# Optimization experiments

Hardware: AMD Instinct MI355X
Metric: run time of the kernel (lower is better)

The kernel has to match this reference:

```python
import jax, jax.numpy as jnp
import numpy as np

F_SIZE = 32
H_DIM = 540
W_DIM = 960
T_DIM = 300
HID1 = 64
FEAT = 64
HID2X2 = 256
UV_L = 10
T_L = 6
BLOCK2_IN = FEAT + (UV_L * 2 * 2 + 2) + (T_L * 2 + 1)  # 119
N_PTS = 1048576


def plane_sample(plane, uv):
    """Bilinear grid_sample, align_corners=False, padding_mode='border'.
    plane: (f, H, W); uv: (N, 2) in [0,1]; uv[:,0] samples W, uv[:,1] samples H
    (matches torch grid last-dim (x, y) convention). Returns (N, f)."""
    f, H, W = plane.shape
    g = uv * 2.0 - 1.0
    u, v = g[:, 0], g[:, 1]
    # unnormalize (align_corners=False) then border-clamp the coordinate
    ix = jnp.clip(((u + 1.0) * W - 1.0) * 0.5, 0.0, W - 1.0)
    iy = jnp.clip(((v + 1.0) * H - 1.0) * 0.5, 0.0, H - 1.0)
    x0f = jnp.floor(ix)
    y0f = jnp.floor(iy)
    wx = ix - x0f
    wy = iy - y0f
    x0 = x0f.astype(jnp.int32)
    y0 = y0f.astype(jnp.int32)
    x1 = jnp.minimum(x0 + 1, W - 1)
    y1 = jnp.minimum(y0 + 1, H - 1)
    v00 = plane[:, y0, x0]  # (f, N)
    v01 = plane[:, y0, x1]
    v10 = plane[:, y1, x0]
    v11 = plane[:, y1, x1]
    out = (v00 * (1 - wx) * (1 - wy) + v01 * wx * (1 - wy)
           + v10 * (1 - wx) * wy + v11 * wx * wy)
    return out.T  # (N, f)


def pos_enc(x, L):
    outs = [x]
    for j in range(L):
        s = (2.0 ** j) * x
        outs.append(jnp.sin(s))
        outs.append(jnp.cos(s))
    return jnp.concatenate(outs, axis=-1)


def _linear_params(key, fan_in, fan_out):
    kw, kb = jax.random.split(key)
    scale = 1.0 / np.sqrt(fan_in)
    W = jax.random.uniform(kw, (fan_in, fan_out), minval=-scale, maxval=scale, dtype=jnp.float32)
    b = jax.random.uniform(kb, (fan_out,), minval=-scale, maxval=scale, dtype=jnp.float32)
    return W, b


def setup_inputs() -> dict:
    key = jax.random.key(0)
    ks = jax.random.split(key, 10)
    xyt = jax.random.uniform(ks[0], (N_PTS, 3), dtype=jnp.float32)
    xyt = xyt.at[:, 2].multiply(300.0)  # t in [0, frames_num)
    yx_plane = jax.random.uniform(ks[1], (F_SIZE, H_DIM, W_DIM), dtype=jnp.float32)
    xt_plane = jax.random.uniform(ks[2], (F_SIZE, W_DIM, T_DIM), dtype=jnp.float32)
    yt_plane = jax.random.uniform(ks[3], (F_SIZE, H_DIM, T_DIM), dtype=jnp.float32)
    fw1, fb1 = _linear_params(ks[4], F_SIZE, HID1)
    fw2, fb2 = _linear_params(ks[5], HID1, FEAT)
    w1, b1 = _linear_params(ks[6], BLOCK2_IN, HID2X2)
    w2, b2 = _linear_params(ks[7], HID2X2, HID2X2)
    w3, b3 = _linear_params(ks[8], HID2X2, HID2X2)
    w4, b4 = _linear_params(ks[9], HID2X2, 3)
    return {"xyt": xyt, "yx_plane": yx_plane, "xt_plane": xt_plane,
            "yt_plane": yt_plane, "fw1": fw1, "fb1": fb1, "fw2": fw2,
            "fb2": fb2, "w1": w1, "b1": b1, "w2": w2, "b2": b2,
            "w3": w3, "b3": b3, "w4": w4, "b4": b4, "frames_num": 300}


def reference(xyt, yx_plane, xt_plane, yt_plane, fw1, fb1, fw2, fb2,
              w1, b1, w2, b2, w3, b3, w4, b4, frames_num):
    x = xyt[:, 0:1]
    y = xyt[:, 1:2]
    t = xyt[:, 2:3] / frames_num
    yx_f = plane_sample(yx_plane, jnp.concatenate([y, x], axis=-1))
    xt_f = plane_sample(xt_plane, jnp.concatenate([x, t], axis=-1))
    yt_f = plane_sample(yt_plane, jnp.concatenate([y, t], axis=-1))
    feat = yx_f * xt_f * yt_f  # (N, f_size)
    h = jax.nn.relu(feat @ fw1 + fb1)
    h = jax.nn.relu(h @ fw2 + fb2)
    yx_pe = pos_enc(jnp.concatenate([y, x], axis=-1), UV_L)
    t_pe = pos_enc(t, T_L)
    full = jnp.concatenate([h, yx_pe, t_pe], axis=-1)  # (N, 119)
    z = jax.nn.relu(full @ w1 + b1)
    z = jax.nn.relu(z @ w2 + b2)
    z = jax.nn.relu(z @ w3 + b3)
    colors = jax.nn.sigmoid(z @ w4 + b4)  # (N, 3)
    return colors
```

## Files before the change

kernel.cpp:

```cpp
#include <hip/hip_runtime.h>

typedef __bf16 bf16_t;
typedef __bf16 bf16x8 __attribute__((ext_vector_type(8)));
typedef _Float16 f16x4 __attribute__((ext_vector_type(4)));
typedef unsigned short u16x8 __attribute__((ext_vector_type(8)));
typedef unsigned short u16x4 __attribute__((ext_vector_type(4)));
typedef float f32x4 __attribute__((ext_vector_type(4)));

#define MT 64
#define NTHR 512
#define NBLK (1048576 / MT)

__device__ __forceinline__ int fragoff(int NK, int pg, int n, int p15) {
  return ((pg * NK + (n >> 5)) << 10) + (((n >> 3) & 3) << 8) + (p15 << 4) + ((n & 7) << 1);
}
__device__ __forceinline__ void st_frag1(char* buf, int NK, int pg, int n, int p15, float v) {
  *reinterpret_cast<unsigned short*>(buf + fragoff(NK, pg, n, p15)) =
      __builtin_bit_cast(unsigned short, (bf16_t)v);
}
__device__ __forceinline__ void st_frag4(char* buf, int NK, int pg, int n, int p15, float v0,
                                         float v1, float v2, float v3) {
  u16x4 pk;
  pk[0] = __builtin_bit_cast(unsigned short, (bf16_t)v0);
  pk[1] = __builtin_bit_cast(unsigned short, (bf16_t)v1);
  pk[2] = __builtin_bit_cast(unsigned short, (bf16_t)v2);
  pk[3] = __builtin_bit_cast(unsigned short, (bf16_t)v3);
  *reinterpret_cast<uint2*>(buf + fragoff(NK, pg, n, p15)) = __builtin_bit_cast(uint2, pk);
}

__global__ void KPlanes_tr3(const float* __restrict__ yx, const float* __restrict__ xt,
                            const float* __restrict__ yt, uint4* __restrict__ d0,
                            uint4* __restrict__ d1, uint4* __restrict__ d2) {
  const int HW0 = 518400, HW1 = 288000, HW2 = 162000;
  const int NB0 = 2025, NB1 = 1125;
  const int b = blockIdx.x;
  const float* src;
  uint4* dst;
  int HW, s;
  if (b < NB0) {
    src = yx; dst = d0; HW = HW0; s = b * 256 + threadIdx.x;
  } else if (b < NB0 + NB1) {
    src = xt; dst = d1; HW = HW1; s = (b - NB0) * 256 + threadIdx.x;
  } else {
    src = yt; dst = d2; HW = HW2; s = (b - NB0 - NB1) * 256 + threadIdx.x;
  }
  if (s >= HW) return;
#pragma unroll
  for (int g = 0; g < 4; ++g) {
    u16x8 v;
#pragma unroll
    for (int j = 0; j < 8; ++j) {
      const float w = src[(size_t)(g * 8 + j) * HW + s];
      v[j] = __builtin_bit_cast(unsigned short, (_Float16)w);
    }
    dst[(size_t)s * 4 + g] = __builtin_bit_cast(uint4, v);
  }
}

__global__ void KPlanes_packall(const float* __restrict__ fw1, const float* __restrict__ fw2,
                                const float* __restrict__ w1, const float* __restrict__ w2,
                                const float* __restrict__ w3, const float* __restrict__ w4,
                                uint4* __restrict__ dst) {
  const int F = blockIdx.x * 4 + (threadIdx.x >> 6);
  const int lane = threadIdx.x & 63;
  if (F >= 340) return;
  const float* W;
  int N, K, KS, fbase;
  if (F < 4)        { W = fw1; N = 64;  K = 32;  KS = 1; fbase = 0; }
  else if (F < 12)  { W = fw2; N = 64;  K = 64;  KS = 2; fbase = 4; }
  else if (F < 76)  { W = w1;  N = 256; K = 119; KS = 4; fbase = 12; }
  else if (F < 204) { W = w2;  N = 256; K = 256; KS = 8; fbase = 76; }
  else if (F < 332) { W = w3;  N = 256; K = 256; KS = 8; fbase = 204; }
  else              { W = w4;  N = 3;   K = 256; KS = 8; fbase = 332; }
  const int f = F - fbase;
  const int g = f / KS, ks = f - g * KS;
  const int col = g * 16 + (lane & 15);
  u16x8 v;
#pragma unroll
  for (int j = 0; j < 8; ++j) {
    const int k = ks * 32 + (lane >> 4) * 8 + j;
    const float w = (k < K && col < N) ? W[(size_t)k * N + col] : 0.0f;
    v[j] = __builtin_bit_cast(unsigned short, (bf16_t)w);
  }
  dst[(size_t)F * 64 + lane] = __builtin_bit_cast(uint4, v);
}

struct Smp4 {
  uint2 c00, c01, c10, c11;
  float w00, w01, w10, w11;
};
__device__ __forceinline__ Smp4 sample_ld4(const uint2* __restrict__ plt, int Hd, int Wd, float u,
                                           float v, int q) {
  Smp4 s;
  float ix = fminf(fmaxf(u * (float)Wd - 0.5f, 0.f), (float)Wd - 1.f);
  float iy = fminf(fmaxf(v * (float)Hd - 0.5f, 0.f), (float)Hd - 1.f);
  float x0f = floorf(ix), y0f = floorf(iy);
  float wx = ix - x0f, wy = iy - y0f;
  int x0 = (int)x0f, y0 = (int)y0f;
  int x1 = min(x0 + 1, Wd - 1), y1 = min(y0 + 1, Hd - 1);
  s.w00 = (1.f - wx) * (1.f - wy);
  s.w01 = wx * (1.f - wy);
  s.w10 = (1.f - wx) * wy;
  s.w11 = wx * wy;
  const size_t r0 = (size_t)y0 * Wd, r1 = (size_t)y1 * Wd;
  s.c00 = plt[(r0 + x0) * 8 + q];
  s.c01 = plt[(r0 + x1) * 8 + q];
  s.c10 = plt[(r1 + x0) * 8 + q];
  s.c11 = plt[(r1 + x1) * 8 + q];
  return s;
}
__device__ __forceinline__ void smp_combine4(const Smp4& s, float* o) {
  const f16x4 a = __builtin_bit_cast(f16x4, s.c00);
  const f16x4 b = __builtin_bit_cast(f16x4, s.c01);
  const f16x4 c = __builtin_bit_cast(f16x4, s.c10);
  const f16x4 d = __builtin_bit_cast(f16x4, s.c11);
#pragma unroll
  for (int i = 0; i < 4; ++i)
    o[i] = (float)a[i] * s.w00 + (float)b[i] * s.w01 + (float)c[i] * s.w10 + (float)d[i] * s.w11;
}

template <int KS, int NKOUT, int NT, int MTPW, bool RELU>
__device__ __forceinline__ void layer_fp(const char* in, char* outb, const uint4* __restrict__ Wf,
                                         const float* __restrict__ bg, int gbase, int moff,
                                         int lane) {
  const int l15 = lane & 15, lhi = lane >> 4;
  const char* rb = in + lane * 16 + moff * (KS << 10);
  f32x4 acc[MTPW][NT];
#pragma unroll
  for (int m = 0; m < MTPW; ++m)
#pragma unroll
    for (int t = 0; t < NT; ++t) acc[m][t] = f32x4{0.f, 0.f, 0.f, 0.f};
#pragma unroll
  for (int ks = 0; ks < KS; ++ks) {
    bf16x8 wa[NT];
#pragma unroll
    for (int t = 0; t < NT; ++t)
      wa[t] = __builtin_bit_cast(bf16x8, Wf[(size_t)((gbase + t) * KS + ks) * 64 + lane]);
#pragma unroll
    for (int m = 0; m < MTPW; ++m) {
      const uint4 u = *reinterpret_cast<const uint4*>(rb + ((m * KS + ks) << 10));
      const bf16x8 b = __builtin_bit_cast(bf16x8, u);
#pragma unroll
      for (int t = 0; t < NT; ++t)
        acc[m][t] = __builtin_amdgcn_mfma_f32_16x16x32_bf16(wa[t], b, acc[m][t], 0, 0, 0);
    }
  }
#pragma unroll
  for (int t = 0; t < NT; ++t) {
    const int ncol = (gbase + t) * 16 + lhi * 4;
    const float4 bb = *reinterpret_cast<const float4*>(&bg[ncol]);
#pragma unroll
    for (int m = 0; m < MTPW; ++m) {
      float v0 = acc[m][t][0] + bb.x, v1 = acc[m][t][1] + bb.y;
      float v2 = acc[m][t][2] + bb.z, v3 = acc[m][t][3] + bb.w;
      if (RELU) {
        v0 = fmaxf(v0, 0.f); v1 = fmaxf(v1, 0.f);
        v2 = fmaxf(v2, 0.f); v3 = fmaxf(v3, 0.f);
      }
      st_frag4(outb, NKOUT, moff + m, ncol, l15, v0, v1, v2, v3);
    }
  }
}

__global__ __launch_bounds__(NTHR, 4) void KPlanes_fused7(
    const float* __restrict__ xyt, const uint2* __restrict__ yx_h, const uint2* __restrict__ xt_h,
    const uint2* __restrict__ yt_h, const uint4* __restrict__ wf1, const float* __restrict__ fb1,
    const uint4* __restrict__ wf2, const float* __restrict__ fb2, const uint4* __restrict__ wf3,
    const float* __restrict__ b1, const uint4* __restrict__ wf4, const float* __restrict__ b2,
    const uint4* __restrict__ wf5, const float* __restrict__ b3, const uint4* __restrict__ wf6,
    const float* __restrict__ b4, const int* __restrict__ fnum_p, float* __restrict__ out) {
  __shared__ char actS[32768];
  __shared__ char actB[32768];
  const int tid = threadIdx.x;
  const int lane = tid & 63;
  const int wid = tid >> 6;
  const float rfn = 1.0f / (float)(*fnum_p);

  {
    const int p = tid >> 3;
    const int q = tid & 7;
    const int pg = p >> 4, p15 = p & 15;
    const int pgl = blockIdx.x * MT + p;
    const float x = xyt[pgl * 3 + 0];
    const float y = xyt[pgl * 3 + 1];
    const float t = xyt[pgl * 3 + 2] * rfn;
    Smp4 sYX = sample_ld4(yx_h, 540, 960, y, x, q);
    Smp4 sXT = sample_ld4(xt_h, 960, 300, x, t, q);
    Smp4 sYT = sample_ld4(yt_h, 540, 300, y, t, q);
    if (q == 4) {
      st_frag1(actS, 4, pg, 64, p15, y);
      float sj, cj;
      sincosf(y, &sj, &cj);
#pragma unroll
      for (int j = 0; j < 10; ++j) {
        st_frag1(actS, 4, pg, 66 + j * 4, p15, sj);
        st_frag1(actS, 4, pg, 68 + j * 4, p15, cj);
        const float ns = 2.f * sj * cj;
        cj = fmaf(-2.f * sj, sj, 1.f);
        sj = ns;
      }
    } else if (q == 5) {
      st_frag1(actS, 4, pg, 65, p15, x);
      float sj, cj;
      sincosf(x, &sj, &cj);
#pragma unroll
      for (int j = 0; j < 10; ++j) {
        st_frag1(actS, 4, pg, 67 + j * 4, p15, sj);
        st_frag1(actS, 4, pg, 69 + j * 4, p15, cj);
        const float ns = 2.f * sj * cj;
        cj = fmaf(-2.f * sj, sj, 1.f);
        sj = ns;
      }
    } else if (q == 6) {
      st_frag1(actS, 4, pg, 106, p15, t);
      float sj, cj;
      sincosf(t, &sj, &cj);
#pragma unroll
      for (int j = 0; j < 6; ++j) {
        st_frag1(actS, 4, pg, 107 + 2 * j, p15, sj);
        st_frag1(actS, 4, pg, 108 + 2 * j, p15, cj);
        const float ns = 2.f * sj * cj;
        cj = fmaf(-2.f * sj, sj, 1.f);
        sj = ns;
      }
    } else if (q == 7) {
      st_frag1(actS, 4, pg, 119, p15, 0.f);
      *reinterpret_cast<uint4*>(actS + fragoff(4, pg, 120, p15)) = uint4{0u, 0u, 0u, 0u};
    }
    float a4[4], b4_[4], c4[4];
    smp_combine4(sYX, a4);
    smp_combine4(sXT, b4_);
    smp_combine4(sYT, c4);
    st_frag4(actS + 16384, 1, pg, q * 4, p15, a4[0] * b4_[0] * c4[0], a4[1] * b4_[1] * c4[1],
             a4[2] * b4_[2] * c4[2], a4[3] * b4_[3] * c4[3]);
  }
  __syncthreads();
  layer_fp<1, 2, 1, 2, true>(actS + 16384, actB, wf1, fb1, wid & 3, (wid >> 2) * 2, lane);
  __syncthreads();
  layer_fp<2, 4, 1, 2, true>(actB, actS, wf2, fb2, wid & 3, (wid >> 2) * 2, lane);
  __syncthreads();
  layer_fp<4, 8, 2, 4, true>(actS, actB, wf3, b1, wid * 2, 0, lane);
  __syncthreads();
  layer_fp<8, 8, 2, 4, true>(actB, actS, wf4, b2, wid * 2, 0, lane);
  __syncthreads();
  layer_fp<8, 8, 2, 4, true>(actS, actB, wf5, b3, wid * 2, 0, lane);
  __syncthreads();
  if (wid < 4) {
    const int l15 = lane & 15, lhi = lane >> 4;
    const char* rb = actB + lane * 16 + wid * 8192;
    f32x4 acc = {0.f, 0.f, 0.f, 0.f};
#pragma unroll
    for (int ks = 0; ks < 8; ++ks) {
      const bf16x8 wa = __builtin_bit_cast(bf16x8, wf6[ks * 64 + lane]);
      const bf16x8 b = __builtin_bit_cast(bf16x8, *reinterpret_cast<const uint4*>(rb + (ks << 10)));
      acc = __builtin_amdgcn_mfma_f32_16x16x32_bf16(wa, b, acc, 0, 0, 0);
    }
    if (lhi == 0) {
      const size_t pgl = (size_t)blockIdx.x * MT + wid * 16 + l15;
#pragma unroll
      for (int i = 0; i < 3; ++i) {
        const float v = acc[i] + b4[i];
        out[pgl * 3 + i] = 1.f / (1.f + expf(-v));
      }
    }
  }
}

__device__ __forceinline__ int swz(int row, int colbyte) {
  return row * 512 + (colbyte ^ ((row & 31) << 4));
}
__device__ __forceinline__ void st_act(unsigned short* buf, int row, int col, float v) {
  buf[swz(row, col * 2) >> 1] = __builtin_bit_cast(unsigned short, (bf16_t)v);
}
__device__ __forceinline__ bf16x8 ld_frag(const unsigned short* buf, int row, int kbyte) {
  const uint4 u =
      *reinterpret_cast<const uint4*>(reinterpret_cast<const char*>(buf) + swz(row, kbyte));
  return __builtin_bit_cast(bf16x8, u);
}
__device__ __forceinline__ void sample8_f(const float* __restrict__ pl, int Hd, int Wd, float u,
                                          float v, int cgrp, float* o) {
  float ix = fminf(fmaxf(u * (float)Wd - 0.5f, 0.f), (float)Wd - 1.f);
  float iy = fminf(fmaxf(v * (float)Hd - 0.5f, 0.f), (float)Hd - 1.f);
  float x0f = floorf(ix), y0f = floorf(iy);
  float wx = ix - x0f, wy = iy - y0f;
  int x0 = (int)x0f, y0 = (int)y0f;
  int x1 = min(x0 + 1, Wd - 1), y1 = min(y0 + 1, Hd - 1);
  float w00 = (1.f - wx) * (1.f - wy), w01 = wx * (1.f - wy);
  float w10 = (1.f - wx) * wy, w11 = wx * wy;
  const size_t HW = (size_t)Hd * Wd;
#pragma unroll
  for (int i = 0; i < 8; ++i) {
    const float* bc = pl + (size_t)(cgrp + i) * HW;
    float a = bc[(size_t)y0 * Wd + x0], b = bc[(size_t)y0 * Wd + x1];
    float c = bc[(size_t)y1 * Wd + x0], d = bc[(size_t)y1 * Wd + x1];
    o[i] = a * w00 + b * w01 + c * w10 + d * w11;
  }
}

template <int KSTEPS, int NCPW, bool RELU>
__device__ __forceinline__ void mfma_layer_fb(const unsigned short* inb, unsigned short* outb,
                                              const float* __restrict__ Wg,
                                              const float* __restrict__ bg, int N, int Kmax,
                                              int wid, int lane) {
  const int l15 = lane & 15;
  const int lhi = lane >> 4;
#pragma unroll
  for (int t = 0; t < NCPW; ++t) {
    const int nc = wid * NCPW + t;
    const int col = nc * 16 + l15;
    const float bias = bg[col];
    bf16x8 bfrag[KSTEPS];
#pragma unroll
    for (int ks = 0; ks < KSTEPS; ++ks) {
#pragma unroll
      for (int j = 0; j < 8; ++j) {
        const int k = ks * 32 + lhi * 8 + j;
        float wv = (k < Kmax) ? Wg[(size_t)k * N + col] : 0.0f;
        bfrag[ks][j] = (bf16_t)wv;
      }
    }
#pragma unroll
    for (int m = 0; m < 4; ++m) {
      f32x4 acc = {0.f, 0.f, 0.f, 0.f};
#pragma unroll
      for (int ks = 0; ks < KSTEPS; ++ks) {
        bf16x8 a = ld_frag(inb, m * 16 + l15, ks * 64 + lhi * 16);
        acc = __builtin_amdgcn_mfma_f32_16x16x32_bf16(a, bfrag[ks], acc, 0, 0, 0);
      }
      const int r0 = m * 16 + lhi * 4;
#pragma unroll
      for (int i = 0; i < 4; ++i) {
        float v = acc[i] + bias;
        if (RELU) v = fmaxf(v, 0.f);
        st_act(outb, r0 + i, col, v);
      }
    }
  }
}

__global__ __launch_bounds__(256) void KPlanes_fused_fb(
    const float* __restrict__ xyt, const float* __restrict__ yx, const float* __restrict__ xt,
    const float* __restrict__ yt, const float* __restrict__ fw1, const float* __restrict__ fb1,
    const float* __restrict__ fw2, const float* __restrict__ fb2, const float* __restrict__ w1,
    const float* __restrict__ b1, const float* __restrict__ w2, const float* __restrict__ b2,
    const float* __restrict__ w3, const float* __restrict__ b3, const float* __restrict__ w4,
    const float* __restrict__ b4, const int* __restrict__ fnum_p, float* __restrict__ out) {
  __shared__ unsigned short actA[64 * 256];
  __shared__ unsigned short actB[64 * 256];
  const int tid = threadIdx.x;
  const int lane = tid & 63;
  const int wid = tid >> 6;
  const float fnum = (float)(*fnum_p);
  {
    const int p = tid >> 2;
    const int cgrp = (tid & 3) * 8;
    const int pg = blockIdx.x * 64 + p;
    float x = xyt[pg * 3 + 0];
    float y = xyt[pg * 3 + 1];
    float t = xyt[pg * 3 + 2] / fnum;
    float syx[8], sxt[8], syt[8];
    sample8_f(yx, 540, 960, y, x, cgrp, syx);
    sample8_f(xt, 960, 300, x, t, cgrp, sxt);
    sample8_f(yt, 540, 300, y, t, cgrp, syt);
#pragma unroll
    for (int i = 0; i < 8; ++i) st_act(actA, p, cgrp + i, syx[i] * sxt[i] * syt[i]);
  }
  __syncthreads();
  mfma_layer_fb<1, 1, true>(actA, actB, fw1, fb1, 64, 32, wid, lane);
  __syncthreads();
  mfma_layer_fb<2, 1, true>(actB, actA, fw2, fb2, 64, 64, wid, lane);
  if (tid < 64) {
    const int pg = blockIdx.x * 64 + tid;
    float px = xyt[pg * 3 + 0];
    float py = xyt[pg * 3 + 1];
    float pt = xyt[pg * 3 + 2] / fnum;
    st_act(actA, tid, 64, py);
    st_act(actA, tid, 65, px);
    float sc = 1.f;
#pragma unroll
    for (int j = 0; j < 10; ++j) {
      st_act(actA, tid, 66 + j * 4 + 0, sinf(sc * py));
      st_act(actA, tid, 66 + j * 4 + 1, sinf(sc * px));
      st_act(actA, tid, 66 + j * 4 + 2, cosf(sc * py));
      st_act(actA, tid, 66 + j * 4 + 3, cosf(sc * px));
      sc *= 2.f;
    }
    st_act(actA, tid, 106, pt);
    sc = 1.f;
#pragma unroll
    for (int j = 0; j < 6; ++j) {
      st_act(actA, tid, 107 + j * 2, sinf(sc * pt));
      st_act(actA, tid, 108 + j * 2, cosf(sc * pt));
      sc *= 2.f;
    }
#pragma unroll
    for (int c = 119; c < 128; ++c) st_act(actA, tid, c, 0.f);
  }
  __syncthreads();
  mfma_layer_fb<4, 4, true>(actA, actB, w1, b1, 256, 119, wid, lane);
  __syncthreads();
  mfma_layer_fb<8, 4, true>(actB, actA, w2, b2, 256, 256, wid, lane);
  __syncthreads();
  mfma_layer_fb<8, 4, true>(actA, actB, w3, b3, 256, 256, wid, lane);
  __syncthreads();
  {
    const int p = tid >> 2, c = tid & 3;
    if (c < 3) {
      float acc = 0.f;
#pragma unroll
      for (int k0 = 0; k0 < 256; k0 += 8) {
        int b = swz(p, k0 * 2);
        uint4 u = *reinterpret_cast<const uint4*>(reinterpret_cast<const char*>(actB) + b);
        bf16x8 z = __builtin_bit_cast(bf16x8, u);
#pragma unroll
        for (int j = 0; j < 8; ++j) acc += (float)z[j] * w4[(k0 + j) * 3 + c];
      }
      acc += b4[c];
      out[(size_t)(blockIdx.x * 64 + p) * 3 + c] = 1.f / (1.f + expf(-acc));
    }
  }
}

extern "C" void kernel_launch(void* const* d_in, const int* in_sizes, int n_in, void* d_out,
                              int out_size, void* d_ws, size_t ws_size, hipStream_t stream) {
  const float* xyt = (const float*)d_in[0];
  const float* yx = (const float*)d_in[1];
  const float* xt = (const float*)d_in[2];
  const float* yt = (const float*)d_in[3];
  const float* fw1 = (const float*)d_in[4];
  const float* fb1 = (const float*)d_in[5];
  const float* fw2 = (const float*)d_in[6];
  const float* fb2 = (const float*)d_in[7];
  const float* w1 = (const float*)d_in[8];
  const float* b1 = (const float*)d_in[9];
  const float* w2 = (const float*)d_in[10];
  const float* b2 = (const float*)d_in[11];
  const float* w3 = (const float*)d_in[12];
  const float* b3 = (const float*)d_in[13];
  const float* w4 = (const float*)d_in[14];
  const float* b4 = (const float*)d_in[15];
  const int* fnum = (const int*)d_in[16];
  float* out = (float*)d_out;

  const int hw_yx = 540 * 960, hw_xt = 960 * 300, hw_yt = 540 * 300;
  const size_t plane_bytes = ((size_t)hw_yx + hw_xt + hw_yt) * 64;
  const size_t wfrag_bytes = (size_t)340 * 64 * sizeof(uint4);
  const size_t need = plane_bytes + wfrag_bytes;

  char* ws = (char*)d_ws;
  uint2* yx_h = (uint2*)ws;
  uint2* xt_h = (uint2*)(ws + (size_t)hw_yx * 64);
  uint2* yt_h = (uint2*)(ws + (size_t)(hw_yx + hw_xt) * 64);
  uint4* wbase = (uint4*)(ws + plane_bytes);
  uint4* wf1 = wbase + 0 * 64;
  uint4* wf2 = wbase + 4 * 64;
  uint4* wf3 = wbase + 12 * 64;
  uint4* wf4 = wbase + 76 * 64;
  uint4* wf5 = wbase + 204 * 64;
  uint4* wf6 = wbase + 332 * 64;

  if (ws_size >= need) {
    const int nb_tr = 2025 + 1125 + 633;
    KPlanes_tr3<<<nb_tr, 256, 0, stream>>>(yx, xt, yt, (uint4*)yx_h, (uint4*)xt_h, (uint4*)yt_h);
    KPlanes_packall<<<85, 256, 0, stream>>>(fw1, fw2, w1, w2, w3, w4, wbase);
    KPlanes_fused7<<<NBLK, NTHR, 0, stream>>>(xyt, yx_h, xt_h, yt_h, wf1, fb1, wf2, fb2, wf3, b1,
                                              wf4, b2, wf5, b3, wf6, b4, fnum, out);
  } else {
    KPlanes_fused_fb<<<1048576 / 64, 256, 0, stream>>>(xyt, yx, xt, yt, fw1, fb1, fw2, fb2, w1,
                                                       b1, w2, b2, w3, b3, w4, b4, fnum, out);
  }
}
```

Before: 477.2 us.

## Halve LDS with in-place MLP layers to raise occupancy

Merges the two 32KB shared activation buffers into one 32KB buffer. The three wide layers now compute in place: each wave accumulates in registers, hits a barrier, then writes its outputs over the input. The work split is also changed so each wave owns one 16-point group and half of the output columns. Launch bounds go from 4 to 6 blocks per CU, trading extra register pressure and more barriers for higher occupancy to hide the latency of the gathers.

```diff
diff --git a/kernel.cpp b/kernel.cpp
--- a/kernel.cpp
+++ b/kernel.cpp
@@ -162,15 +162,49 @@
   }
 }
 
-__global__ __launch_bounds__(NTHR, 4) void KPlanes_fused7(
+template <int KS, bool RELU>
+__device__ __forceinline__ void layer_ipf(char* Zb, int inoff, const uint4* __restrict__ Wf,
+                                          const float* __restrict__ bg, int wid, int lane) {
+  const int l15 = lane & 15, lhi = lane >> 4;
+  const int pg = wid >> 1, nh = wid & 1;
+  const char* rb = Zb + inoff + pg * (KS << 10) + lane * 16;
+  const uint4* wp = Wf + (size_t)(nh * 8) * KS * 64 + lane;
+  f32x4 acc[8];
+#pragma unroll
+  for (int t = 0; t < 8; ++t) acc[t] = f32x4{0.f, 0.f, 0.f, 0.f};
+#pragma unroll
+  for (int ks = 0; ks < KS; ++ks) {
+    const bf16x8 b = __builtin_bit_cast(bf16x8, *reinterpret_cast<const uint4*>(rb + (ks << 10)));
+#pragma unroll
+    for (int t = 0; t < 8; ++t) {
+      const bf16x8 wa = __builtin_bit_cast(bf16x8, wp[(size_t)(t * KS + ks) * 64]);
+      acc[t] = __builtin_amdgcn_mfma_f32_16x16x32_bf16(wa, b, acc[t], 0, 0, 0);
+    }
+  }
+  __syncthreads();
+#pragma unroll
+  for (int t = 0; t < 8; ++t) {
+    const int ncol = (nh * 8 + t) * 16 + lhi * 4;
+    const float4 bb = *reinterpret_cast<const float4*>(&bg[ncol]);
+    float v0 = acc[t][0] + bb.x, v1 = acc[t][1] + bb.y;
+    float v2 = acc[t][2] + bb.z, v3 = acc[t][3] + bb.w;
+    if (RELU) {
+      v0 = fmaxf(v0, 0.f); v1 = fmaxf(v1, 0.f);
+      v2 = fmaxf(v2, 0.f); v3 = fmaxf(v3, 0.f);
+    }
+    st_frag4(Zb, 8, pg, ncol, l15, v0, v1, v2, v3);
+  }
+  __syncthreads();
+}
+
+__global__ __launch_bounds__(NTHR, 6) void KPlanes_fused8(
     const float* __restrict__ xyt, const uint2* __restrict__ yx_h, const uint2* __restrict__ xt_h,
     const uint2* __restrict__ yt_h, const uint4* __restrict__ wf1, const float* __restrict__ fb1,
     const uint4* __restrict__ wf2, const float* __restrict__ fb2, const uint4* __restrict__ wf3,
     const float* __restrict__ b1, const uint4* __restrict__ wf4, const float* __restrict__ b2,
     const uint4* __restrict__ wf5, const float* __restrict__ b3, const uint4* __restrict__ wf6,
     const float* __restrict__ b4, const int* __restrict__ fnum_p, float* __restrict__ out) {
-  __shared__ char actS[32768];
-  __shared__ char actB[32768];
+  __shared__ char Z[32768];
   const int tid = threadIdx.x;
   const int lane = tid & 63;
   const int wid = tid >> 6;
@@ -187,67 +221,65 @@
     Smp4 sYX = sample_ld4(yx_h, 540, 960, y, x, q);
     Smp4 sXT = sample_ld4(xt_h, 960, 300, x, t, q);
     Smp4 sYT = sample_ld4(yt_h, 540, 300, y, t, q);
+    char* pe = Z + 8192;
     if (q == 4) {
-      st_frag1(actS, 4, pg, 64, p15, y);
+      st_frag1(pe, 4, pg, 64, p15, y);
       float sj, cj;
       sincosf(y, &sj, &cj);
 #pragma unroll
       for (int j = 0; j < 10; ++j) {
-        st_frag1(actS, 4, pg, 66 + j * 4, p15, sj);
-        st_frag1(actS, 4, pg, 68 + j * 4, p15, cj);
+        st_frag1(pe, 4, pg, 66 + j * 4, p15, sj);
+        st_frag1(pe, 4, pg, 68 + j * 4, p15, cj);
         const float ns = 2.f * sj * cj;
         cj = fmaf(-2.f * sj, sj, 1.f);
         sj = ns;
       }
     } else if (q == 5) {
-      st_frag1(actS, 4, pg, 65, p15, x);
+      st_frag1(pe, 4, pg, 65, p15, x);
       float sj, cj;
       sincosf(x, &sj, &cj);
 #pragma unroll
       for (int j = 0; j < 10; ++j) {
-        st_frag1(actS, 4, pg, 67 + j * 4, p15, sj);
-        st_frag1(actS, 4, pg, 69 + j * 4, p15, cj);
+        st_frag1(pe, 4, pg, 67 + j * 4, p15, sj);
+        st_frag1(pe, 4, pg, 69 + j * 4, p15, cj);
         const float ns = 2.f * sj * cj;
         cj = fmaf(-2.f * sj, sj, 1.f);
         sj = ns;
       }
     } else if (q == 6) {
-      st_frag1(actS, 4, pg, 106, p15, t);
+      st_frag1(pe, 4, pg, 106, p15, t);
       float sj, cj;
       sincosf(t, &sj, &cj);
 #pragma unroll
       for (int j = 0; j < 6; ++j) {
-        st_frag1(actS, 4, pg, 107 + 2 * j, p15, sj);
-        st_frag1(actS, 4, pg, 108 + 2 * j, p15, cj);
+        st_frag1(pe, 4, pg, 107 + 2 * j, p15, sj);
+        st_frag1(pe, 4, pg, 108 + 2 * j, p15, cj);
         const float ns = 2.f * sj * cj;
         cj = fmaf(-2.f * sj, sj, 1.f);
         sj = ns;
       }
     } else if (q == 7) {
-      st_frag1(actS, 4, pg, 119, p15, 0.f);
-      *reinterpret_cast<uint4*>(actS + fragoff(4, pg, 120, p15)) = uint4{0u, 0u, 0u, 0u};
+      st_frag1(pe, 4, pg, 119, p15, 0.f);
+      *reinterpret_cast<uint4*>(pe + fragoff(4, pg, 120, p15)) = uint4{0u, 0u, 0u, 0u};
     }
     float a4[4], b4_[4], c4[4];
     smp_combine4(sYX, a4);
     smp_combine4(sXT, b4_);
     smp_combine4(sYT, c4);
-    st_frag4(actS + 16384, 1, pg, q * 4, p15, a4[0] * b4_[0] * c4[0], a4[1] * b4_[1] * c4[1],
+    st_frag4(Z + 28672, 1, pg, q * 4, p15, a4[0] * b4_[0] * c4[0], a4[1] * b4_[1] * c4[1],
              a4[2] * b4_[2] * c4[2], a4[3] * b4_[3] * c4[3]);
   }
   __syncthreads();
-  layer_fp<1, 2, 1, 2, true>(actS + 16384, actB, wf1, fb1, wid & 3, (wid >> 2) * 2, lane);
-  __syncthreads();
-  layer_fp<2, 4, 1, 2, true>(actB, actS, wf2, fb2, wid & 3, (wid >> 2) * 2, lane);
-  __syncthreads();
-  layer_fp<4, 8, 2, 4, true>(actS, actB, wf3, b1, wid * 2, 0, lane);
-  __syncthreads();
-  layer_fp<8, 8, 2, 4, true>(actB, actS, wf4, b2, wid * 2, 0, lane);
-  __syncthreads();
-  layer_fp<8, 8, 2, 4, true>(actS, actB, wf5, b3, wid * 2, 0, lane);
-  __syncthreads();
+  layer_fp<1, 2, 1, 2, true>(Z + 28672, Z, wf1, fb1, wid & 3, (wid >> 2) * 2, lane);
+  __syncthreads();
+  layer_fp<2, 4, 1, 2, true>(Z, Z + 8192, wf2, fb2, wid & 3, (wid >> 2) * 2, lane);
+  __syncthreads();
+  layer_ipf<4, true>(Z, 8192, wf3, b1, wid, lane);
+  layer_ipf<8, true>(Z, 0, wf4, b2, wid, lane);
+  layer_ipf<8, true>(Z, 0, wf5, b3, wid, lane);
   if (wid < 4) {
     const int l15 = lane & 15, lhi = lane >> 4;
-    const char* rb = actB + lane * 16 + wid * 8192;
+    const char* rb = Z + lane * 16 + wid * 8192;
     f32x4 acc = {0.f, 0.f, 0.f, 0.f};
 #pragma unroll
     for (int ks = 0; ks < 8; ++ks) {
@@ -463,7 +495,7 @@
     const int nb_tr = 2025 + 1125 + 633;
     KPlanes_tr3<<<nb_tr, 256, 0, stream>>>(yx, xt, yt, (uint4*)yx_h, (uint4*)xt_h, (uint4*)yt_h);
     KPlanes_packall<<<85, 256, 0, stream>>>(fw1, fw2, w1, w2, w3, w4, wbase);
-    KPlanes_fused7<<<NBLK, NTHR, 0, stream>>>(xyt, yx_h, xt_h, yt_h, wf1, fb1, wf2, fb2, wf3, b1,
+    KPlanes_fused8<<<NBLK, NTHR, 0, stream>>>(xyt, yx_h, xt_h, yt_h, wf1, fb1, wf2, fb2, wf3, b1,
                                               wf4, b2, wf5, b3, wf6, b4, fnum, out);
   } else {
     KPlanes_fused_fb<<<1048576 / 64, 256, 0, stream>>>(xyt, yx, xt, yt, fw1, fb1, fw2, fb2, w1,
```

Measured after the change: 1.227 ms. +157.2%, slower.

## Make fused kernel loop over tiles and prefetch next tile's plane samples

Applied to the files above, without the earlier changes.

The fused kernel becomes semi-persistent: each block processes 32 consecutive 64-point tiles instead of one. It issues the plane gathers for the next tile, and the coordinate loads for the tile after that, before running the current tile's MLP layers. The aim is to hide gather latency behind the MFMA work and to amortize block launch and setup. In exchange the grid drops to 512 blocks, which may leave CU slots idle given the 4-blocks-per-CU launch bound. Holding the sample state across the layers also adds register pressure.

```diff
diff --git a/kernel.cpp b/kernel.cpp
--- a/kernel.cpp
+++ b/kernel.cpp
@@ -9,7 +9,8 @@
 
 #define MT 64
 #define NTHR 512
-#define NBLK (1048576 / MT)
+#define TPB 32
+#define NPBLK (1048576 / (MT * TPB))
 
 __device__ __forceinline__ int fragoff(int NK, int pg, int n, int p15) {
   return ((pg * NK + (n >> 5)) << 10) + (((n >> 3) & 3) << 8) + (p15 << 4) + ((n & 7) << 1);
@@ -162,7 +163,7 @@
   }
 }
 
-__global__ __launch_bounds__(NTHR, 4) void KPlanes_fused7(
+__global__ __launch_bounds__(NTHR, 4) void KPlanes_fusedP(
     const float* __restrict__ xyt, const uint2* __restrict__ yx_h, const uint2* __restrict__ xt_h,
     const uint2* __restrict__ yt_h, const uint4* __restrict__ wf1, const float* __restrict__ fb1,
     const uint4* __restrict__ wf2, const float* __restrict__ fb2, const uint4* __restrict__ wf3,
@@ -175,18 +176,37 @@
   const int lane = tid & 63;
   const int wid = tid >> 6;
   const float rfn = 1.0f / (float)(*fnum_p);
-
+  const int p = tid >> 3, q = tid & 7;
+  const int pg = p >> 4, p15 = p & 15;
+  const int tbase = blockIdx.x * TPB;
+
+  float x, y, t, xn, yn, tn;
   {
-    const int p = tid >> 3;
-    const int q = tid & 7;
-    const int pg = p >> 4, p15 = p & 15;
-    const int pgl = blockIdx.x * MT + p;
-    const float x = xyt[pgl * 3 + 0];
-    const float y = xyt[pgl * 3 + 1];
-    const float t = xyt[pgl * 3 + 2] * rfn;
-    Smp4 sYX = sample_ld4(yx_h, 540, 960, y, x, q);
-    Smp4 sXT = sample_ld4(xt_h, 960, 300, x, t, q);
-    Smp4 sYT = sample_ld4(yt_h, 540, 300, y, t, q);
+    const int p0 = tbase * MT + p;
+    x = xyt[p0 * 3 + 0];
+    y = xyt[p0 * 3 + 1];
+    t = xyt[p0 * 3 + 2] * rfn;
+  }
+  Smp4 sYX = sample_ld4(yx_h, 540, 960, y, x, q);
+  Smp4 sXT = sample_ld4(xt_h, 960, 300, x, t, q);
+  Smp4 sYT = sample_ld4(yt_h, 540, 300, y, t, q);
+  {
+    const int p1 = (tbase + 1) * MT + p;
+    xn = xyt[p1 * 3 + 0];
+    yn = xyt[p1 * 3 + 1];
+    tn = xyt[p1 * 3 + 2] * rfn;
+  }
+
+#pragma unroll 1
+  for (int it = 0; it < TPB; ++it) {
+    {
+      float a4[4], b4_[4], c4[4];
+      smp_combine4(sYX, a4);
+      smp_combine4(sXT, b4_);
+      smp_combine4(sYT, c4);
+      st_frag4(actS + 16384, 1, pg, q * 4, p15, a4[0] * b4_[0] * c4[0], a4[1] * b4_[1] * c4[1],
+               a4[2] * b4_[2] * c4[2], a4[3] * b4_[3] * c4[3]);
+    }
     if (q == 4) {
       st_frag1(actS, 4, pg, 64, p15, y);
       float sj, cj;
@@ -227,42 +247,52 @@
       st_frag1(actS, 4, pg, 119, p15, 0.f);
       *reinterpret_cast<uint4*>(actS + fragoff(4, pg, 120, p15)) = uint4{0u, 0u, 0u, 0u};
     }
-    float a4[4], b4_[4], c4[4];
-    smp_combine4(sYX, a4);
-    smp_combine4(sXT, b4_);
-    smp_combine4(sYT, c4);
-    st_frag4(actS + 16384, 1, pg, q * 4, p15, a4[0] * b4_[0] * c4[0], a4[1] * b4_[1] * c4[1],
-             a4[2] * b4_[2] * c4[2], a4[3] * b4_[3] * c4[3]);
-  }
-  __syncthreads();
-  layer_fp<1, 2, 1, 2, true>(actS + 16384, actB, wf1, fb1, wid & 3, (wid >> 2) * 2, lane);
-  __syncthreads();
-  layer_fp<2, 4, 1, 2, true>(actB, actS, wf2, fb2, wid & 3, (wid >> 2) * 2, lane);
-  __syncthreads();
-  layer_fp<4, 8, 2, 4, true>(actS, actB, wf3, b1, wid * 2, 0, lane);
-  __syncthreads();
-  layer_fp<8, 8, 2, 4, true>(actB, actS, wf4, b2, wid * 2, 0, lane);
-  __syncthreads();
-  layer_fp<8, 8, 2, 4, true>(actS, actB, wf5, b3, wid * 2, 0, lane);
-  __syncthreads();
-  if (wid < 4) {
-    const int l15 = lane & 15, lhi = lane >> 4;
-    const char* rb = actB + lane * 16 + wid * 8192;
-    f32x4 acc = {0.f, 0.f, 0.f, 0.f};
-#pragma unroll
-    for (int ks = 0; ks < 8; ++ks) {
-      const bf16x8 wa = __builtin_bit_cast(bf16x8, wf6[ks * 64 + lane]);
-      const bf16x8 b = __builtin_bit_cast(bf16x8, *reinterpret_cast<const uint4*>(rb + (ks << 10)));
-      acc = __builtin_amdgcn_mfma_f32_16x16x32_bf16(wa, b, acc, 0, 0, 0);
-    }
-    if (lhi == 0) {
-      const size_t pgl = (size_t)blockIdx.x * MT + wid * 16 + l15;
-#pragma unroll
-      for (int i = 0; i < 3; ++i) {
-        const float v = acc[i] + b4[i];
-        out[pgl * 3 + i] = 1.f / (1.f + expf(-v));
-      }
-    }
+    if (it + 1 < TPB) {
+      sYX = sample_ld4(yx_h, 540, 960, yn, xn, q);
+      sXT = sample_ld4(xt_h, 960, 300, xn, tn, q);
+      sYT = sample_ld4(yt_h, 540, 300, yn, tn, q);
+    }
+    float xn2, yn2, tn2;
+    {
+      const int it2 = (it + 2 < TPB) ? (it + 2) : (TPB - 1);
+      const int p2 = (tbase + it2) * MT + p;
+      xn2 = xyt[p2 * 3 + 0];
+      yn2 = xyt[p2 * 3 + 1];
+      tn2 = xyt[p2 * 3 + 2] * rfn;
+    }
+    __syncthreads();
+    layer_fp<1, 2, 1, 2, true>(actS + 16384, actB, wf1, fb1, wid & 3, (wid >> 2) * 2, lane);
+    __syncthreads();
+    layer_fp<2, 4, 1, 2, true>(actB, actS, wf2, fb2, wid & 3, (wid >> 2) * 2, lane);
+    __syncthreads();
+    layer_fp<4, 8, 2, 4, true>(actS, actB, wf3, b1, wid * 2, 0, lane);
+    __syncthreads();
+    layer_fp<8, 8, 2, 4, true>(actB, actS, wf4, b2, wid * 2, 0, lane);
+    __syncthreads();
+    layer_fp<8, 8, 2, 4, true>(actS, actB, wf5, b3, wid * 2, 0, lane);
+    __syncthreads();
+    if (wid < 4) {
+      const int l15 = lane & 15, lhi = lane >> 4;
+      const char* rb = actB + lane * 16 + wid * 8192;
+      f32x4 acc = {0.f, 0.f, 0.f, 0.f};
+#pragma unroll
+      for (int ks = 0; ks < 8; ++ks) {
+        const bf16x8 wa = __builtin_bit_cast(bf16x8, wf6[ks * 64 + lane]);
+        const bf16x8 b =
+            __builtin_bit_cast(bf16x8, *reinterpret_cast<const uint4*>(rb + (ks << 10)));
+        acc = __builtin_amdgcn_mfma_f32_16x16x32_bf16(wa, b, acc, 0, 0, 0);
+      }
+      if (lhi == 0) {
+        const size_t pgl = (size_t)(tbase + it) * MT + wid * 16 + l15;
+#pragma unroll
+        for (int i = 0; i < 3; ++i) {
+          const float v = acc[i] + b4[i];
+          out[pgl * 3 + i] = 1.f / (1.f + expf(-v));
+        }
+      }
+    }
+    x = xn; y = yn; t = tn;
+    xn = xn2; yn = yn2; tn = tn2;
   }
 }
 
@@ -463,8 +493,8 @@
     const int nb_tr = 2025 + 1125 + 633;
     KPlanes_tr3<<<nb_tr, 256, 0, stream>>>(yx, xt, yt, (uint4*)yx_h, (uint4*)xt_h, (uint4*)yt_h);
     KPlanes_packall<<<85, 256, 0, stream>>>(fw1, fw2, w1, w2, w3, w4, wbase);
-    KPlanes_fused7<<<NBLK, NTHR, 0, stream>>>(xyt, yx_h, xt_h, yt_h, wf1, fb1, wf2, fb2, wf3, b1,
-                                              wf4, b2, wf5, b3, wf6, b4, fnum, out);
+    KPlanes_fusedP<<<NPBLK, NTHR, 0, stream>>>(xyt, yx_h, xt_h, yt_h, wf1, fb1, wf2, fb2, wf3, b1,
+                                               wf4, b2, wf5, b3, wf6, b4, fnum, out);
   } else {
     KPlanes_fused_fb<<<1048576 / 64, 256, 0, stream>>>(xyt, yx, xt, yt, fw1, fb1, fw2, fb2, w1,
                                                        b1, w2, b2, w3, b3, w4, b4, fnum, out);
```

Result: slower. 1.826 ms (+282.7%).
